# Kernel tuning notes

Hardware: AMD Instinct MI355X
Metric: run time of the kernel (lower is better)

## Reference

```python
import jax, jax.numpy as jnp
import numpy as np

N_CLUSTERS = 512
TEMPERATURE = 0.1


def setup_inputs() -> dict:
    key = jax.random.key(0)
    k1, k2 = jax.random.split(key)
    x = jax.random.normal(k1, (32, 1024, 256), dtype=jnp.float32)
    centroids = jax.random.normal(k2, (N_CLUSTERS, 256), dtype=jnp.float32)
    return {"x": x, "centroids": centroids}


def reference(x, centroids):
    # Flatten non-cluster axes into a sample axis: [N, D]
    B, S, D = x.shape
    xf = x.reshape(-1, D)  # [N, D]
    x_sq = jnp.sum(xf * xf, axis=-1, keepdims=True)           # [N, 1]
    c_sq = jnp.sum(centroids * centroids, axis=-1)             # [K]
    cross = jnp.einsum('nd,kd->nk', xf, centroids)             # [N, K]
    dists = x_sq - 2.0 * cross + c_sq[None, :]                 # [N, K]
    # Temperature-scaled soft assignments
    assignments = jax.nn.softmax(-dists / TEMPERATURE, axis=-1)  # [N, K]
    # Restore leading (non-feature) dims, append cluster axis
    return assignments.reshape(B, S, N_CLUSTERS)
```

## Files before the change

kernel.cpp:

```cpp
#include <hip/hip_runtime.h>

#define NROWS 32768
#define KC 512
#define DDIM 256
#define BM 128
#define BK 32
#define KCH (DDIM / BK)
#define CHUNK_USH (KC * BK)

typedef __attribute__((ext_vector_type(8))) short bf16x8;
typedef __attribute__((ext_vector_type(4))) float f32x4;

union U8 { unsigned short u[8]; bf16x8 v; };

__device__ __forceinline__ unsigned short f2bf(float f) {
    union { float f; unsigned int u; } a; a.f = f;
    unsigned int r = a.u + 0x7fffu + ((a.u >> 16) & 1u);
    return (unsigned short)(r >> 16);
}
__device__ __forceinline__ float bf2f(unsigned short h) {
    union { unsigned int u; float f; } a; a.u = ((unsigned int)h) << 16;
    return a.f;
}
__device__ __forceinline__ void ld16(const void* g, void* l) {
    __builtin_amdgcn_global_load_lds(
        (const __attribute__((address_space(1))) unsigned int*)g,
        (__attribute__((address_space(3))) unsigned int*)l, 16, 0, 0);
}

__global__ __launch_bounds__(64) void prep_c(const float* __restrict__ c,
                                             unsigned short* __restrict__ bhi,
                                             unsigned short* __restrict__ blo,
                                             float* __restrict__ csq10) {
    const int n = blockIdx.x, lane = threadIdx.x;
    const int d0 = lane * 4;
    float4 v = ((const float4*)(c + (size_t)n * DDIM))[lane];
    float vv[4] = {v.x, v.y, v.z, v.w};
    unsigned short hh[4], ll[4];
    float ssq = 0.f;
    #pragma unroll
    for (int i = 0; i < 4; ++i) {
        ssq += vv[i] * vv[i];
        hh[i] = f2bf(vv[i]);
        ll[i] = f2bf(vv[i] - bf2f(hh[i]));
    }
    #pragma unroll
    for (int off = 32; off; off >>= 1) ssq += __shfl_xor(ssq, off);
    if (lane == 0) csq10[n] = 10.f * ssq;
    const int ks = d0 >> 5;
    const int q  = (d0 >> 3) & 3;
    const int s  = q ^ ((n >> 1) & 3);
    const size_t dst = (size_t)ks * CHUNK_USH + (n * 4 + s) * 8 + (d0 & 7);
    *(ushort4*)(bhi + dst) = make_ushort4(hh[0], hh[1], hh[2], hh[3]);
    *(ushort4*)(blo + dst) = make_ushort4(ll[0], ll[1], ll[2], ll[3]);
}

union SmemU {
    struct { unsigned short Bh[2][CHUNK_USH], Bl[2][CHUNK_USH]; } k;
    float lbuf[32 * 516];
};

__global__ __launch_bounds__(512, 2) void kmeans_mfma(
    const float* __restrict__ x, const unsigned short* __restrict__ bhi,
    const unsigned short* __restrict__ blo, const float* __restrict__ csq10,
    float* __restrict__ out) {
    __shared__ __align__(16) SmemU sm;
    __shared__ float  red0[4][BM], red1[4][BM];
    __shared__ float2 MI[BM];

    const int tid  = threadIdx.x;
    const int w    = tid >> 6, lane = tid & 63;
    const int wm   = w >> 2, wn = w & 3;
    const int cc   = lane & 15, q = lane >> 4;
    const int row0 = blockIdx.x * BM;

    f32x4 acc[4][8];
    #pragma unroll
    for (int mt = 0; mt < 4; ++mt)
        #pragma unroll
        for (int t = 0; t < 8; ++t) acc[mt][t] = (f32x4){0.f, 0.f, 0.f, 0.f};

    const float* xA[4];
    #pragma unroll
    for (int mt = 0; mt < 4; ++mt)
        xA[mt] = x + (size_t)(row0 + wm * 64 + mt * 16 + cc) * DDIM + q * 8;
    const int sF = q ^ ((cc >> 1) & 3);
    const int bF = (4 * cc + sF) * 8;
    const int dmaOff = (w * 4) * 512;

    #pragma unroll
    for (int j = 0; j < 4; ++j) {
        const int o = dmaOff + j * 512;
        ld16(bhi + o + lane * 8, &sm.k.Bh[0][o]);
        ld16(blo + o + lane * 8, &sm.k.Bl[0][o]);
    }
    float4 a[4][2];
    #pragma unroll
    for (int mt = 0; mt < 4; ++mt) {
        a[mt][0] = *(const float4*)(xA[mt]);
        a[mt][1] = *(const float4*)(xA[mt] + 4);
    }
    __syncthreads();

    for (int ks = 0; ks < KCH; ++ks) {
        const int pp = ks & 1;
        float4 n[4][2];
        if (ks < KCH - 1) {
            const size_t cb = (size_t)(ks + 1) * CHUNK_USH;
            #pragma unroll
            for (int j = 0; j < 4; ++j) {
                const int o = dmaOff + j * 512;
                ld16(bhi + cb + o + lane * 8, &sm.k.Bh[1 - pp][o]);
                ld16(blo + cb + o + lane * 8, &sm.k.Bl[1 - pp][o]);
            }
            const int kn = (ks + 1) * BK;
            #pragma unroll
            for (int mt = 0; mt < 4; ++mt) {
                n[mt][0] = *(const float4*)(xA[mt] + kn);
                n[mt][1] = *(const float4*)(xA[mt] + kn + 4);
            }
        }
        bf16x8 ah[4], al[4];
        #pragma unroll
        for (int mt = 0; mt < 4; ++mt) {
            float v8[8] = {a[mt][0].x, a[mt][0].y, a[mt][0].z, a[mt][0].w,
                           a[mt][1].x, a[mt][1].y, a[mt][1].z, a[mt][1].w};
            U8 H, L;
            #pragma unroll
            for (int i = 0; i < 8; ++i) {
                H.u[i] = f2bf(v8[i]);
                L.u[i] = f2bf(v8[i] - bf2f(H.u[i]));
            }
            ah[mt] = H.v; al[mt] = L.v;
        }
        #pragma unroll
        for (int t = 0; t < 8; ++t) {
            const int bo = (wn * 8 + t) * 512 + bF;
            bf16x8 bh = *(const bf16x8*)&sm.k.Bh[pp][bo];
            bf16x8 bl = *(const bf16x8*)&sm.k.Bl[pp][bo];
            #pragma unroll
            for (int mt = 0; mt < 4; ++mt) {
                acc[mt][t] = __builtin_amdgcn_mfma_f32_16x16x32_bf16(ah[mt], bh, acc[mt][t], 0, 0, 0);
                acc[mt][t] = __builtin_amdgcn_mfma_f32_16x16x32_bf16(ah[mt], bl, acc[mt][t], 0, 0, 0);
                acc[mt][t] = __builtin_amdgcn_mfma_f32_16x16x32_bf16(al[mt], bh, acc[mt][t], 0, 0, 0);
            }
        }
        #pragma unroll
        for (int mt = 0; mt < 4; ++mt) { a[mt][0] = n[mt][0]; a[mt][1] = n[mt][1]; }
        __syncthreads();
    }

    float csqv[8];
    #pragma unroll
    for (int t = 0; t < 8; ++t) csqv[t] = csq10[wn * 128 + t * 16 + cc];

    #pragma unroll
    for (int mt = 0; mt < 4; ++mt)
        #pragma unroll
        for (int g = 0; g < 4; ++g) {
            float pm = -1e30f;
            #pragma unroll
            for (int t = 0; t < 8; ++t) pm = fmaxf(pm, 20.f * acc[mt][t][g] - csqv[t]);
            #pragma unroll
            for (int off = 1; off < 16; off <<= 1) pm = fmaxf(pm, __shfl_xor(pm, off));
            if (cc == 0) red0[wn][wm * 64 + mt * 16 + q * 4 + g] = pm;
        }
    __syncthreads();
    float M[4][4];
    #pragma unroll
    for (int mt = 0; mt < 4; ++mt)
        #pragma unroll
        for (int g = 0; g < 4; ++g) {
            const int row = wm * 64 + mt * 16 + q * 4 + g;
            float Mf = fmaxf(fmaxf(red0[0][row], red0[1][row]),
                             fmaxf(red0[2][row], red0[3][row]));
            M[mt][g] = Mf;
            float ps = 0.f;
            #pragma unroll
            for (int t = 0; t < 8; ++t) ps += __expf(20.f * acc[mt][t][g] - csqv[t] - Mf);
            #pragma unroll
            for (int off = 1; off < 16; off <<= 1) ps += __shfl_xor(ps, off);
            if (cc == 0) red1[wn][row] = ps;
        }
    __syncthreads();
    if (tid < BM) {
        const float Mf = fmaxf(fmaxf(red0[0][tid], red0[1][tid]),
                               fmaxf(red0[2][tid], red0[3][tid]));
        const float Sf = red1[0][tid] + red1[1][tid] + red1[2][tid] + red1[3][tid];
        MI[tid] = make_float2(Mf, 1.f / Sf);
    }
    __syncthreads();

    #pragma unroll
    for (int p = 0; p < 4; ++p) {
        if (wm == (p >> 1)) {
            #pragma unroll
            for (int mi = 0; mi < 2; ++mi) {
                const int mt = (p & 1) * 2 + mi;
                #pragma unroll
                for (int g = 0; g < 4; ++g) {
                    const int    lr  = mi * 16 + q * 4 + g;
                    const float2 mi2 = MI[p * 32 + lr];
                    #pragma unroll
                    for (int t = 0; t < 8; ++t)
                        sm.lbuf[lr * 516 + wn * 128 + t * 16 + cc] =
                            __expf(20.f * acc[mt][t][g] - csqv[t] - mi2.x) * mi2.y;
                }
            }
        }
        __syncthreads();
        #pragma unroll
        for (int j = 0; j < 8; ++j) {
            const int f    = j * 512 + tid;
            const int lrow = f >> 7;
            const int c4   = f & 127;
            float4    v    = *(const float4*)&sm.lbuf[lrow * 516 + c4 * 4];
            *(float4*)(out + (size_t)(row0 + p * 32 + lrow) * KC + c4 * 4) = v;
        }
        __syncthreads();
    }
}

extern "C" void kernel_launch(void* const* d_in, const int* in_sizes, int n_in,
                              void* d_out, int out_size, void* d_ws, size_t ws_size,
                              hipStream_t stream) {
    const float* x   = (const float*)d_in[0];
    const float* c   = (const float*)d_in[1];
    float*       out = (float*)d_out;

    unsigned short* bhi   = (unsigned short*)d_ws;
    unsigned short* blo   = bhi + (size_t)KCH * CHUNK_USH;
    float*          csq10 = (float*)(blo + (size_t)KCH * CHUNK_USH);

    prep_c<<<KC, 64, 0, stream>>>(c, bhi, blo, csq10);
    kmeans_mfma<<<NROWS / BM, 512, 0, stream>>>(x, bhi, blo, csq10, out);
}
```

Baseline: 129.0 us.

## Stage bf16-split X tile in LDS and repartition warps across centroid columns

```diff
diff --git a/kernel.cpp b/kernel.cpp
--- a/kernel.cpp
+++ b/kernel.cpp
@@ -7,6 +7,7 @@
 #define BK 32
 #define KCH (DDIM / BK)
 #define CHUNK_USH (KC * BK)
+#define ASTR 40
 
 typedef __attribute__((ext_vector_type(8))) short bf16x8;
 typedef __attribute__((ext_vector_type(4))) float f32x4;
@@ -57,7 +58,12 @@
 
 union SmemU {
     struct { unsigned short Bh[2][CHUNK_USH], Bl[2][CHUNK_USH]; } k;
-    float lbuf[32 * 516];
+    struct {
+        float  lbuf[32 * 516];
+        float  red0[8][BM];
+        float  red1[8][BM];
+        float2 MI[BM];
+    } e;
 };
 
 __global__ __launch_bounds__(512, 2) void kmeans_mfma(
@@ -65,28 +71,27 @@
     const unsigned short* __restrict__ blo, const float* __restrict__ csq10,
     float* __restrict__ out) {
     __shared__ __align__(16) SmemU sm;
-    __shared__ float  red0[4][BM], red1[4][BM];
-    __shared__ float2 MI[BM];
+    __shared__ __align__(16) unsigned short Ah[BM * ASTR], Al[BM * ASTR];
 
     const int tid  = threadIdx.x;
-    const int w    = tid >> 6, lane = tid & 63;
-    const int wm   = w >> 2, wn = w & 3;
+    const int wn   = tid >> 6, lane = tid & 63;
     const int cc   = lane & 15, q = lane >> 4;
     const int row0 = blockIdx.x * BM;
 
-    f32x4 acc[4][8];
-    #pragma unroll
-    for (int mt = 0; mt < 4; ++mt)
-        #pragma unroll
-        for (int t = 0; t < 8; ++t) acc[mt][t] = (f32x4){0.f, 0.f, 0.f, 0.f};
-
-    const float* xA[4];
-    #pragma unroll
-    for (int mt = 0; mt < 4; ++mt)
-        xA[mt] = x + (size_t)(row0 + wm * 64 + mt * 16 + cc) * DDIM + q * 8;
+    f32x4 acc[8][4];
+    #pragma unroll
+    for (int mt = 0; mt < 8; ++mt)
+        #pragma unroll
+        for (int t = 0; t < 4; ++t) acc[mt][t] = (f32x4){0.f, 0.f, 0.f, 0.f};
+
+    const int       sRow = tid >> 2, sOct = tid & 3;
+    const float*    xg   = x + (size_t)(row0 + sRow) * DDIM + sOct * 8;
+    unsigned short* aHiW = &Ah[sRow * ASTR + sOct * 8];
+    unsigned short* aLoW = &Al[sRow * ASTR + sOct * 8];
+
     const int sF = q ^ ((cc >> 1) & 3);
     const int bF = (4 * cc + sF) * 8;
-    const int dmaOff = (w * 4) * 512;
+    const int dmaOff = (wn * 4) * 512;
 
     #pragma unroll
     for (int j = 0; j < 4; ++j) {
@@ -94,17 +99,24 @@
         ld16(bhi + o + lane * 8, &sm.k.Bh[0][o]);
         ld16(blo + o + lane * 8, &sm.k.Bl[0][o]);
     }
-    float4 a[4][2];
-    #pragma unroll
-    for (int mt = 0; mt < 4; ++mt) {
-        a[mt][0] = *(const float4*)(xA[mt]);
-        a[mt][1] = *(const float4*)(xA[mt] + 4);
+    {
+        float4 p0 = *(const float4*)xg;
+        float4 p1 = *(const float4*)(xg + 4);
+        float v8[8] = {p0.x, p0.y, p0.z, p0.w, p1.x, p1.y, p1.z, p1.w};
+        U8 H, L;
+        #pragma unroll
+        for (int i = 0; i < 8; ++i) {
+            H.u[i] = f2bf(v8[i]);
+            L.u[i] = f2bf(v8[i] - bf2f(H.u[i]));
+        }
+        *(bf16x8*)aHiW = H.v;
+        *(bf16x8*)aLoW = L.v;
     }
     __syncthreads();
 
     for (int ks = 0; ks < KCH; ++ks) {
         const int pp = ks & 1;
-        float4 n[4][2];
+        float4 p0, p1;
         if (ks < KCH - 1) {
             const size_t cb = (size_t)(ks + 1) * CHUNK_USH;
             #pragma unroll
@@ -113,99 +125,101 @@
                 ld16(bhi + cb + o + lane * 8, &sm.k.Bh[1 - pp][o]);
                 ld16(blo + cb + o + lane * 8, &sm.k.Bl[1 - pp][o]);
             }
-            const int kn = (ks + 1) * BK;
-            #pragma unroll
-            for (int mt = 0; mt < 4; ++mt) {
-                n[mt][0] = *(const float4*)(xA[mt] + kn);
-                n[mt][1] = *(const float4*)(xA[mt] + kn + 4);
-            }
-        }
-        bf16x8 ah[4], al[4];
-        #pragma unroll
-        for (int mt = 0; mt < 4; ++mt) {
-            float v8[8] = {a[mt][0].x, a[mt][0].y, a[mt][0].z, a[mt][0].w,
-                           a[mt][1].x, a[mt][1].y, a[mt][1].z, a[mt][1].w};
+            p0 = *(const float4*)(xg + (ks + 1) * BK);
+            p1 = *(const float4*)(xg + (ks + 1) * BK + 4);
+        }
+        bf16x8 bh[4], bl[4];
+        #pragma unroll
+        for (int t = 0; t < 4; ++t) {
+            const int bo = (wn * 4 + t) * 512 + bF;
+            bh[t] = *(const bf16x8*)&sm.k.Bh[pp][bo];
+            bl[t] = *(const bf16x8*)&sm.k.Bl[pp][bo];
+        }
+        #pragma unroll
+        for (int mt = 0; mt < 8; ++mt) {
+            const int ao = (mt * 16 + cc) * ASTR + q * 8;
+            bf16x8 ah = *(const bf16x8*)&Ah[ao];
+            bf16x8 al = *(const bf16x8*)&Al[ao];
+            #pragma unroll
+            for (int t = 0; t < 4; ++t) {
+                acc[mt][t] = __builtin_amdgcn_mfma_f32_16x16x32_bf16(ah, bh[t], acc[mt][t], 0, 0, 0);
+                acc[mt][t] = __builtin_amdgcn_mfma_f32_16x16x32_bf16(ah, bl[t], acc[mt][t], 0, 0, 0);
+                acc[mt][t] = __builtin_amdgcn_mfma_f32_16x16x32_bf16(al, bh[t], acc[mt][t], 0, 0, 0);
+            }
+        }
+        __syncthreads();
+        if (ks < KCH - 1) {
+            float v8[8] = {p0.x, p0.y, p0.z, p0.w, p1.x, p1.y, p1.z, p1.w};
             U8 H, L;
             #pragma unroll
             for (int i = 0; i < 8; ++i) {
                 H.u[i] = f2bf(v8[i]);
                 L.u[i] = f2bf(v8[i] - bf2f(H.u[i]));
             }
-            ah[mt] = H.v; al[mt] = L.v;
-        }
-        #pragma unroll
-        for (int t = 0; t < 8; ++t) {
-            const int bo = (wn * 8 + t) * 512 + bF;
-            bf16x8 bh = *(const bf16x8*)&sm.k.Bh[pp][bo];
-            bf16x8 bl = *(const bf16x8*)&sm.k.Bl[pp][bo];
-            #pragma unroll
-            for (int mt = 0; mt < 4; ++mt) {
-                acc[mt][t] = __builtin_amdgcn_mfma_f32_16x16x32_bf16(ah[mt], bh, acc[mt][t], 0, 0, 0);
-                acc[mt][t] = __builtin_amdgcn_mfma_f32_16x16x32_bf16(ah[mt], bl, acc[mt][t], 0, 0, 0);
-                acc[mt][t] = __builtin_amdgcn_mfma_f32_16x16x32_bf16(al[mt], bh, acc[mt][t], 0, 0, 0);
-            }
-        }
-        #pragma unroll
-        for (int mt = 0; mt < 4; ++mt) { a[mt][0] = n[mt][0]; a[mt][1] = n[mt][1]; }
-        __syncthreads();
-    }
-
-    float csqv[8];
-    #pragma unroll
-    for (int t = 0; t < 8; ++t) csqv[t] = csq10[wn * 128 + t * 16 + cc];
-
-    #pragma unroll
-    for (int mt = 0; mt < 4; ++mt)
+            *(bf16x8*)aHiW = H.v;
+            *(bf16x8*)aLoW = L.v;
+        }
+        __syncthreads();
+    }
+
+    float csqv[4];
+    #pragma unroll
+    for (int t = 0; t < 4; ++t) csqv[t] = csq10[wn * 64 + t * 16 + cc];
+
+    #pragma unroll
+    for (int mt = 0; mt < 8; ++mt)
         #pragma unroll
         for (int g = 0; g < 4; ++g) {
             float pm = -1e30f;
             #pragma unroll
-            for (int t = 0; t < 8; ++t) pm = fmaxf(pm, 20.f * acc[mt][t][g] - csqv[t]);
+            for (int t = 0; t < 4; ++t) pm = fmaxf(pm, 20.f * acc[mt][t][g] - csqv[t]);
             #pragma unroll
             for (int off = 1; off < 16; off <<= 1) pm = fmaxf(pm, __shfl_xor(pm, off));
-            if (cc == 0) red0[wn][wm * 64 + mt * 16 + q * 4 + g] = pm;
-        }
-    __syncthreads();
-    float M[4][4];
-    #pragma unroll
-    for (int mt = 0; mt < 4; ++mt)
+            if (cc == 0) sm.e.red0[wn][mt * 16 + q * 4 + g] = pm;
+        }
+    __syncthreads();
+    if (tid < BM) {
+        float m = -1e30f;
+        #pragma unroll
+        for (int ww = 0; ww < 8; ++ww) m = fmaxf(m, sm.e.red0[ww][tid]);
+        sm.e.MI[tid].x = m;
+    }
+    __syncthreads();
+    #pragma unroll
+    for (int mt = 0; mt < 8; ++mt)
         #pragma unroll
         for (int g = 0; g < 4; ++g) {
-            const int row = wm * 64 + mt * 16 + q * 4 + g;
-            float Mf = fmaxf(fmaxf(red0[0][row], red0[1][row]),
-                             fmaxf(red0[2][row], red0[3][row]));
-            M[mt][g] = Mf;
+            const int   row = mt * 16 + q * 4 + g;
+            const float Mf  = sm.e.MI[row].x;
             float ps = 0.f;
             #pragma unroll
-            for (int t = 0; t < 8; ++t) ps += __expf(20.f * acc[mt][t][g] - csqv[t] - Mf);
+            for (int t = 0; t < 4; ++t) ps += __expf(20.f * acc[mt][t][g] - csqv[t] - Mf);
             #pragma unroll
             for (int off = 1; off < 16; off <<= 1) ps += __shfl_xor(ps, off);
-            if (cc == 0) red1[wn][row] = ps;
+            if (cc == 0) sm.e.red1[wn][row] = ps;
         }
     __syncthreads();
     if (tid < BM) {
-        const float Mf = fmaxf(fmaxf(red0[0][tid], red0[1][tid]),
-                               fmaxf(red0[2][tid], red0[3][tid]));
-        const float Sf = red1[0][tid] + red1[1][tid] + red1[2][tid] + red1[3][tid];
-        MI[tid] = make_float2(Mf, 1.f / Sf);
+        float s = 0.f;
+        #pragma unroll
+        for (int ww = 0; ww < 8; ++ww) s += sm.e.red1[ww][tid];
+        sm.e.MI[tid].y = 1.f / s;
     }
     __syncthreads();
 
     #pragma unroll
     for (int p = 0; p < 4; ++p) {
-        if (wm == (p >> 1)) {
-            #pragma unroll
-            for (int mi = 0; mi < 2; ++mi) {
-                const int mt = (p & 1) * 2 + mi;
+        #pragma unroll
+        for (int mi = 0; mi < 2; ++mi) {
+            const int mt = p * 2 + mi;
+            #pragma unroll
+            for (int g = 0; g < 4; ++g) {
+                const int    lr = mi * 16 + q * 4 + g;
+                const float2 mv = sm.e.MI[p * 32 + lr];
                 #pragma unroll
-                for (int g = 0; g < 4; ++g) {
-                    const int    lr  = mi * 16 + q * 4 + g;
-                    const float2 mi2 = MI[p * 32 + lr];
-                    #pragma unroll
-                    for (int t = 0; t < 8; ++t)
-                        sm.lbuf[lr * 516 + wn * 128 + t * 16 + cc] =
-                            __expf(20.f * acc[mt][t][g] - csqv[t] - mi2.x) * mi2.y;
-                }
+                for (int t = 0; t < 4; ++t)
+                    sm.e.lbuf[lr * 516 + wn * 64 + t * 16 + cc] =
+                        __expf(20.f * acc[mt][t][g] - csqv[t] - mv.x) * mv.y;
             }
         }
         __syncthreads();
@@ -214,7 +228,7 @@
             const int f    = j * 512 + tid;
             const int lrow = f >> 7;
             const int c4   = f & 127;
-            float4    v    = *(const float4*)&sm.lbuf[lrow * 516 + c4 * 4];
+            float4    v    = *(const float4*)&sm.e.lbuf[lrow * 516 + c4 * 4];
             *(float4*)(out + (size_t)(row0 + p * 32 + lrow) * KC + c4 * 4) = v;
         }
         __syncthreads();
```

Measured after the change: 122.8 us. 1.05x faster.
